# Kernel optimization log

Measured on AMD Instinct MI355X. Metric: run time of the kernel, lower is better.

## Reference

```python
import jax, jax.numpy as jnp
import numpy as np

H = 1024      # hidden_size
I = 2 * H     # intermediate_size (expand_factor=2)
N = 16        # ssm_state_size
K = 4         # conv_kernel
BATCH = 2
SEQ = 2048


def setup_inputs() -> dict:
    key = jax.random.key(0)
    k = jax.random.split(key, 6)
    x = jax.random.normal(k[0], (BATCH, SEQ, H), dtype=jnp.float32)
    # nn.Linear default init ~ U(-1/sqrt(fan_in), 1/sqrt(fan_in)); scale is fine for a reference
    W_in = jax.random.normal(k[1], (2 * I, H), dtype=jnp.float32) / np.sqrt(H)
    conv_w = jax.random.normal(k[2], (I, 1, K), dtype=jnp.float32) / np.sqrt(K)
    W_x = jax.random.normal(k[3], (2 * N + 1, I), dtype=jnp.float32) / np.sqrt(I)
    A_log = jax.random.normal(k[4], (I, N), dtype=jnp.float32)
    D = jnp.ones((I,), dtype=jnp.float32)
    W_out = jax.random.normal(k[5], (H, I), dtype=jnp.float32) / np.sqrt(I)
    return {"x": x, "W_in": W_in, "conv_w": conv_w, "W_x": W_x,
            "A_log": A_log, "D": D, "W_out": W_out}


def reference(x, W_in, conv_w, W_x, A_log, D, W_out):
    xz = jnp.einsum('bsh,ih->bsi', x, W_in)
    xp, z = jnp.split(xz, 2, axis=-1)
    # depthwise causal conv1d: pad left K-1 (torch pads both sides then slices [:S])
    xc = jax.lax.conv_general_dilated(
        xp.transpose(0, 2, 1),           # (B, I, S)
        conv_w,                          # (I, 1, K) = OIH with groups=I
        window_strides=(1,),
        padding=[(K - 1, 0)],
        feature_group_count=I,
        dimension_numbers=('NCH', 'OIH', 'NCH'),
    ).transpose(0, 2, 1)                 # (B, S, I)
    xc = jax.nn.silu(xc)
    # x_proj -> delta (1), B (N), C (N)
    xproj = jnp.einsum('bsi,pi->bsp', xc, W_x)   # (B,S,2N+1)
    delta = jax.nn.softplus(xproj[..., :1])       # (B,S,1)
    Bmat = xproj[..., 1:1 + N]                    # (B,S,N)
    Cmat = xproj[..., 1 + N:]                     # (B,S,N)
    A = -jnp.exp(A_log)                           # (I,N)
    # decay/states broadcast-reduce: (B,S,I,N) intermediates reduced over N
    decay = jnp.exp(delta[..., None] * A[None, None])            # (B,S,I,N)
    states = xc[..., None] * Bmat[:, :, None, :] * decay          # (B,S,I,N)
    y = jnp.sum(states * Cmat[:, :, None, :], axis=-1)            # (B,S,I)
    y = y + xc * D[None, None, :]
    return jnp.einsum('bsi,hi->bsh', y * jax.nn.silu(z), W_out)
```

## Files before the change

kernel.cpp:

```cpp
#include <hip/hip_runtime.h>

#define LOG2E 1.4426950408889634f

__device__ __forceinline__ float b2f(unsigned short u) {
    unsigned int v = ((unsigned int)u) << 16;
    return __builtin_bit_cast(float, v);
}
__device__ __forceinline__ unsigned short f2b(float f) {
    unsigned int u = __builtin_bit_cast(unsigned int, f);
    u += 0x7fffu + ((u >> 16) & 1u);
    return (unsigned short)(u >> 16);
}
__device__ __forceinline__ float fexp(float x) {
    return __builtin_amdgcn_exp2f(x * LOG2E);
}
__device__ __forceinline__ float silu_f(float x) {
    return x * __builtin_amdgcn_rcpf(1.0f + fexp(-x));
}

typedef const __attribute__((address_space(1))) unsigned int* gas_t;
typedef __attribute__((address_space(3))) unsigned int* las_t;
__device__ __forceinline__ void gl2lds16(const unsigned short* g, unsigned short* l) {
    __builtin_amdgcn_global_load_lds((gas_t)(const void*)g, (las_t)(void*)l, 16, 0, 0);
}

__global__ __launch_bounds__(256) void cvt_all_k(const float* __restrict__ x,
                                                 const float* __restrict__ W_in,
                                                 const float* __restrict__ W_out,
                                                 const float* __restrict__ W_x,
                                                 unsigned short* __restrict__ xb,
                                                 unsigned short* __restrict__ wib,
                                                 unsigned short* __restrict__ wob,
                                                 unsigned short* __restrict__ wxb) {
    int b = blockIdx.x;
    const float* src;
    unsigned short* dst;
    if (b < 4096)       { src = x;     dst = xb;  }
    else if (b < 8192)  { src = W_in;  dst = wib; b -= 4096; }
    else if (b < 10240) { src = W_out; dst = wob; b -= 8192; }
    else                { src = W_x;   dst = wxb; b -= 10240; }
    int i = b * 256 + threadIdx.x;
    float4 v = ((const float4*)src)[i];
    *(ushort4*)(dst + (size_t)i * 4) = make_ushort4(f2b(v.x), f2b(v.y), f2b(v.z), f2b(v.w));
}

typedef __bf16 bf16x8 __attribute__((ext_vector_type(8)));
typedef float  fx4    __attribute__((ext_vector_type(4)));
typedef int    ix4    __attribute__((ext_vector_type(4)));
union FragU { ix4 i; bf16x8 b; };

template <bool OUT_BF16>
__global__ __launch_bounds__(256) void gemm_bt(const unsigned short* __restrict__ A,
                                               const unsigned short* __restrict__ B,
                                               void* __restrict__ C, int N, int K) {
    __shared__ __align__(16) unsigned short sA[128 * 64];
    __shared__ __align__(16) unsigned short sB[128 * 64];
    const int tid  = threadIdx.x;
    const int lane = tid & 63, wave = tid >> 6;
    const int bm = blockIdx.y * 128, bn = blockIdx.x * 128;
    const int wm = (wave >> 1) * 64, wn = (wave & 1) * 64;
    const int row16 = lane & 15, quad = lane >> 4;
    const int srow = lane >> 3;
    const int sc16 = (lane & 7) ^ srow;
    const unsigned short* gA = A + (size_t)(bm + wave * 32 + srow) * K + sc16 * 8;
    const unsigned short* gB = B + (size_t)(bn + wave * 32 + srow) * K + sc16 * 8;
    unsigned short* lA = sA + (wave * 4) * 512;
    unsigned short* lB = sB + (wave * 4) * 512;
    fx4 acc[4][4] = {};

    for (int kt = 0; kt < K; kt += 64) {
#pragma unroll
        for (int it = 0; it < 4; ++it) {
            gl2lds16(gA + (size_t)it * 8 * K + kt, lA + it * 512);
            gl2lds16(gB + (size_t)it * 8 * K + kt, lB + it * 512);
        }
        __syncthreads();
#pragma unroll
        for (int kk = 0; kk < 64; kk += 32) {
            FragU af[4], bf[4];
#pragma unroll
            for (int t = 0; t < 4; ++t) {
                int ra = wm + t * 16 + row16;
                af[t].i = *(const ix4*)(sA + ra * 64 + ((quad + (kk >> 3)) ^ (ra & 7)) * 8);
            }
#pragma unroll
            for (int t = 0; t < 4; ++t) {
                int rb = wn + t * 16 + row16;
                bf[t].i = *(const ix4*)(sB + rb * 64 + ((quad + (kk >> 3)) ^ (rb & 7)) * 8);
            }
#pragma unroll
            for (int tm = 0; tm < 4; ++tm)
#pragma unroll
                for (int tn = 0; tn < 4; ++tn)
                    acc[tm][tn] = __builtin_amdgcn_mfma_f32_16x16x32_bf16(
                        af[tm].b, bf[tn].b, acc[tm][tn], 0, 0, 0);
        }
        __syncthreads();
    }
#pragma unroll
    for (int tm = 0; tm < 4; ++tm) {
        int row0 = bm + wm + tm * 16 + quad * 4;
#pragma unroll
        for (int tn = 0; tn < 4; ++tn) {
            int col = bn + wn + tn * 16 + row16;
#pragma unroll
            for (int r = 0; r < 4; ++r) {
                float v = acc[tm][tn][r];
                if (OUT_BF16)
                    ((unsigned short*)C)[(size_t)(row0 + r) * N + col] = f2b(v);
                else
                    ((float*)C)[(size_t)(row0 + r) * N + col] = v;
            }
        }
    }
}

__global__ __launch_bounds__(256) void gemm_bt_n64(const unsigned short* __restrict__ A,
                                                   const unsigned short* __restrict__ B,
                                                   float* __restrict__ C, int N, int K) {
    __shared__ __align__(16) unsigned short sA[128 * 64];
    __shared__ __align__(16) unsigned short sB[64 * 64];
    const int tid  = threadIdx.x;
    const int lane = tid & 63, wave = tid >> 6;
    const int bm = blockIdx.y * 128, bn = blockIdx.x * 64;
    const int wm = wave * 32;
    const int row16 = lane & 15, quad = lane >> 4;
    const int srow = lane >> 3;
    const int sc16 = (lane & 7) ^ srow;
    const unsigned short* gA = A + (size_t)(bm + wave * 32 + srow) * K + sc16 * 8;
    const unsigned short* gB = B + (size_t)(bn + wave * 16 + srow) * K + sc16 * 8;
    unsigned short* lA = sA + (wave * 4) * 512;
    unsigned short* lB = sB + (wave * 2) * 512;
    fx4 acc[2][4] = {};

    for (int kt = 0; kt < K; kt += 64) {
#pragma unroll
        for (int it = 0; it < 4; ++it)
            gl2lds16(gA + (size_t)it * 8 * K + kt, lA + it * 512);
#pragma unroll
        for (int it = 0; it < 2; ++it)
            gl2lds16(gB + (size_t)it * 8 * K + kt, lB + it * 512);
        __syncthreads();
#pragma unroll
        for (int kk = 0; kk < 64; kk += 32) {
            FragU af[2], bf[4];
#pragma unroll
            for (int t = 0; t < 2; ++t) {
                int ra = wm + t * 16 + row16;
                af[t].i = *(const ix4*)(sA + ra * 64 + ((quad + (kk >> 3)) ^ (ra & 7)) * 8);
            }
#pragma unroll
            for (int t = 0; t < 4; ++t) {
                int rb = t * 16 + row16;
                bf[t].i = *(const ix4*)(sB + rb * 64 + ((quad + (kk >> 3)) ^ (rb & 7)) * 8);
            }
#pragma unroll
            for (int tm = 0; tm < 2; ++tm)
#pragma unroll
                for (int tn = 0; tn < 4; ++tn)
                    acc[tm][tn] = __builtin_amdgcn_mfma_f32_16x16x32_bf16(
                        af[tm].b, bf[tn].b, acc[tm][tn], 0, 0, 0);
        }
        __syncthreads();
    }
#pragma unroll
    for (int tm = 0; tm < 2; ++tm) {
        int row0 = bm + wm + tm * 16 + quad * 4;
#pragma unroll
        for (int tn = 0; tn < 4; ++tn) {
            int col = bn + tn * 16 + row16;
#pragma unroll
            for (int r = 0; r < 4; ++r)
                C[(size_t)(row0 + r) * N + col] = acc[tm][tn][r];
        }
    }
}

__global__ __launch_bounds__(256) void fused_mid_k(const unsigned short* __restrict__ xz,
                                                   const float* __restrict__ cw,
                                                   const unsigned short* __restrict__ wxb,
                                                   const float* __restrict__ Alog,
                                                   const float* __restrict__ Dv,
                                                   unsigned short* __restrict__ y2) {
    __shared__ __align__(16) unsigned short sxc[16 * 2048];
    __shared__ float sX[4][16][49];
    __shared__ float sdg[16 * 17];
    const int tid  = threadIdx.x;
    const int lane = tid & 63, wave = tid >> 6;
    const int row16 = lane & 15, quad = lane >> 4;
    const int m0 = blockIdx.x * 16;

    {
        const float4* cw4 = (const float4*)cw;
        float w[8][4];
#pragma unroll
        for (int c = 0; c < 8; ++c) {
            float4 t4 = cw4[tid * 8 + c];
            w[c][0] = t4.x; w[c][1] = t4.y; w[c][2] = t4.z; w[c][3] = t4.w;
        }
        for (int j = 0; j < 16; ++j) {
            const int m = m0 + j, s = m & 2047;
            float acc[8] = {0, 0, 0, 0, 0, 0, 0, 0};
#pragma unroll
            for (int k = 0; k < 4; ++k) {
                if (s - 3 + k >= 0) {
                    const unsigned short* p = xz + (size_t)(m - 3 + k) * 4096 + tid * 8;
                    ushort4 a = *(const ushort4*)p;
                    ushort4 b = *(const ushort4*)(p + 4);
                    float v[8] = {b2f(a.x), b2f(a.y), b2f(a.z), b2f(a.w),
                                  b2f(b.x), b2f(b.y), b2f(b.z), b2f(b.w)};
#pragma unroll
                    for (int c = 0; c < 8; ++c) acc[c] += v[c] * w[c][k];
                }
            }
            unsigned short* q = sxc + j * 2048 + ((tid ^ (j & 7)) * 8);
            *(ushort4*)q       = make_ushort4(f2b(silu_f(acc[0])), f2b(silu_f(acc[1])),
                                              f2b(silu_f(acc[2])), f2b(silu_f(acc[3])));
            *(ushort4*)(q + 4) = make_ushort4(f2b(silu_f(acc[4])), f2b(silu_f(acc[5])),
                                              f2b(silu_f(acc[6])), f2b(silu_f(acc[7])));
        }
    }
    __syncthreads();

    {
        fx4 acc[3] = {};
        const unsigned short* bp = wxb + (size_t)row16 * 2048 + wave * 512 + quad * 8;
        const int cbase = wave * 64 + quad;
#pragma unroll 4
        for (int kk = 0; kk < 512; kk += 32) {
            FragU a, b0, b1, b2;
            int c16 = cbase + (kk >> 3);
            a.i  = *(const ix4*)(sxc + row16 * 2048 + ((c16 ^ (row16 & 7)) * 8));
            b0.i = *(const ix4*)(bp + kk);
            b1.i = *(const ix4*)(bp + 16 * 2048 + kk);
            b2.i = *(const ix4*)(bp + 32 * 2048 + kk);
            acc[0] = __builtin_amdgcn_mfma_f32_16x16x32_bf16(a.b, b0.b, acc[0], 0, 0, 0);
            acc[1] = __builtin_amdgcn_mfma_f32_16x16x32_bf16(a.b, b1.b, acc[1], 0, 0, 0);
            acc[2] = __builtin_amdgcn_mfma_f32_16x16x32_bf16(a.b, b2.b, acc[2], 0, 0, 0);
        }
#pragma unroll
        for (int t = 0; t < 3; ++t)
#pragma unroll
            for (int r = 0; r < 4; ++r)
                sX[wave][quad * 4 + r][t * 16 + row16] = acc[t][r];
    }
    __syncthreads();
    for (int idx = tid; idx < 272; idx += 256) {
        int rr = idx / 17, q = idx - rr * 17;
        float o;
        if (q == 0) {
            float v = sX[0][rr][0] + sX[1][rr][0] + sX[2][rr][0] + sX[3][rr][0];
            o = (v > 20.f) ? v : log1pf(fexp(v));
        } else {
            float bs = sX[0][rr][q]      + sX[1][rr][q]      + sX[2][rr][q]      + sX[3][rr][q];
            float cs = sX[0][rr][q + 16] + sX[1][rr][q + 16] + sX[2][rr][q + 16] + sX[3][rr][q + 16];
            o = bs * cs;
        }
        sdg[rr * 17 + q] = o;
    }
    __syncthreads();

#pragma unroll 1
    for (int p = 0; p < 2; ++p) {
        const int ch0 = p * 1024 + tid * 4;
        float a2[4][16];
#pragma unroll
        for (int c = 0; c < 4; ++c) {
            const float4* ar = (const float4*)(Alog + (size_t)(ch0 + c) * 16);
#pragma unroll
            for (int n4 = 0; n4 < 4; ++n4) {
                float4 t4 = ar[n4];
                a2[c][n4 * 4 + 0] = -fexp(t4.x) * LOG2E;
                a2[c][n4 * 4 + 1] = -fexp(t4.y) * LOG2E;
                a2[c][n4 * 4 + 2] = -fexp(t4.z) * LOG2E;
                a2[c][n4 * 4 + 3] = -fexp(t4.w) * LOG2E;
            }
        }
        float4 dvv = *(const float4*)(Dv + ch0);
        float dv[4] = {dvv.x, dvv.y, dvv.z, dvv.w};
        const int c16 = ch0 >> 3, sub = ch0 & 7;
        for (int j = 0; j < 16; ++j) {
            const int m = m0 + j;
            float delta = sdg[j * 17];
            float Gr[16];
#pragma unroll
            for (int n = 0; n < 16; ++n) Gr[n] = sdg[j * 17 + 1 + n];
            ushort4 xu = *(const ushort4*)(sxc + j * 2048 + ((c16 ^ (j & 7)) * 8) + sub);
            ushort4 zu = *(const ushort4*)(xz + (size_t)m * 4096 + 2048 + ch0);
            float xcv[4] = {b2f(xu.x), b2f(xu.y), b2f(xu.z), b2f(xu.w)};
            float zv[4]  = {b2f(zu.x), b2f(zu.y), b2f(zu.z), b2f(zu.w)};
            unsigned short ov[4];
#pragma unroll
            for (int c = 0; c < 4; ++c) {
                float ssum = 0.f;
#pragma unroll
                for (int n = 0; n < 16; ++n)
                    ssum += Gr[n] * __builtin_amdgcn_exp2f(delta * a2[c][n]);
                float y = xcv[c] * (dv[c] + ssum);
                ov[c] = f2b(y * silu_f(zv[c]));
            }
            *(ushort4*)(y2 + (size_t)m * 2048 + ch0) = make_ushort4(ov[0], ov[1], ov[2], ov[3]);
        }
    }
}

extern "C" void kernel_launch(void* const* d_in, const int* in_sizes, int n_in,
                              void* d_out, int out_size, void* d_ws, size_t ws_size,
                              hipStream_t stream) {
    const float* x      = (const float*)d_in[0];
    const float* W_in   = (const float*)d_in[1];
    const float* conv_w = (const float*)d_in[2];
    const float* W_x    = (const float*)d_in[3];
    const float* A_log  = (const float*)d_in[4];
    const float* Dvec   = (const float*)d_in[5];
    const float* W_out  = (const float*)d_in[6];

    char* ws = (char*)d_ws;
    unsigned short* xb  = (unsigned short*)(ws);
    unsigned short* wib = (unsigned short*)(ws + 8388608);
    unsigned short* wob = (unsigned short*)(ws + 16777216);
    unsigned short* xz  = (unsigned short*)(ws + 20971520);
    unsigned short* y2  = (unsigned short*)(ws + 54525952);
    unsigned short* wxb = (unsigned short*)(ws + 71303168);

    cvt_all_k<<<10306, 256, 0, stream>>>(x, W_in, W_out, W_x, xb, wib, wob, wxb);
    gemm_bt<true><<<dim3(32, 32), 256, 0, stream>>>(xb, wib, xz, 4096, 1024);
    fused_mid_k<<<256, 256, 0, stream>>>(xz, conv_w, wxb, A_log, Dvec, y2);
    gemm_bt_n64<<<dim3(16, 32), 256, 0, stream>>>(y2, wob, (float*)d_out, 1024, 2048);
}
```

Before: 217.9 us.

## Shrink fused mid kernel tile to 4 rows and launch 1024 blocks

The fused conv/x_proj/scan kernel now processes 4 tokens per block instead of 16, cutting LDS use and launching 1024 blocks so more blocks fit per CU and the GPU's CUs are filled (256 blocks was about one per CU). The conv input rows are loaded once into registers as a 7-row window and reused across the 4 outputs, and z loads are hoisted ahead of the scan loop. The tradeoff is that each block re-reads the full W_x matrix for the x_proj MFMA, with only 4 of 16 MFMA rows carrying useful data, and A_log exps are recomputed four times as often.

```diff
diff --git a/kernel.cpp b/kernel.cpp
--- a/kernel.cpp
+++ b/kernel.cpp
@@ -176,21 +176,30 @@
     }
 }
 
-__global__ __launch_bounds__(256) void fused_mid_k(const unsigned short* __restrict__ xz,
-                                                   const float* __restrict__ cw,
-                                                   const unsigned short* __restrict__ wxb,
-                                                   const float* __restrict__ Alog,
-                                                   const float* __restrict__ Dv,
-                                                   unsigned short* __restrict__ y2) {
-    __shared__ __align__(16) unsigned short sxc[16 * 2048];
+__global__ __launch_bounds__(256, 4) void fused_mid_k(const unsigned short* __restrict__ xz,
+                                                      const float* __restrict__ cw,
+                                                      const unsigned short* __restrict__ wxb,
+                                                      const float* __restrict__ Alog,
+                                                      const float* __restrict__ Dv,
+                                                      unsigned short* __restrict__ y2) {
+    __shared__ __align__(16) unsigned short sxc[4 * 2048];
     __shared__ float sX[4][16][49];
-    __shared__ float sdg[16 * 17];
+    __shared__ float sdg[4 * 17];
     const int tid  = threadIdx.x;
     const int lane = tid & 63, wave = tid >> 6;
     const int row16 = lane & 15, quad = lane >> 4;
-    const int m0 = blockIdx.x * 16;
+    const int m0 = blockIdx.x * 4;
 
     {
+        const int s0 = m0 & 2047;
+        ushort4 ua[7], ub[7];
+#pragma unroll
+        for (int t = 0; t < 7; ++t) {
+            int mr = (s0 - 3 + t >= 0) ? (m0 - 3 + t) : m0;
+            const unsigned short* p = xz + (size_t)mr * 4096 + tid * 8;
+            ua[t] = *(const ushort4*)p;
+            ub[t] = *(const ushort4*)(p + 4);
+        }
         const float4* cw4 = (const float4*)cw;
         float w[8][4];
 #pragma unroll
@@ -198,22 +207,28 @@
             float4 t4 = cw4[tid * 8 + c];
             w[c][0] = t4.x; w[c][1] = t4.y; w[c][2] = t4.z; w[c][3] = t4.w;
         }
-        for (int j = 0; j < 16; ++j) {
-            const int m = m0 + j, s = m & 2047;
-            float acc[8] = {0, 0, 0, 0, 0, 0, 0, 0};
-#pragma unroll
-            for (int k = 0; k < 4; ++k) {
-                if (s - 3 + k >= 0) {
-                    const unsigned short* p = xz + (size_t)(m - 3 + k) * 4096 + tid * 8;
-                    ushort4 a = *(const ushort4*)p;
-                    ushort4 b = *(const ushort4*)(p + 4);
-                    float v[8] = {b2f(a.x), b2f(a.y), b2f(a.z), b2f(a.w),
-                                  b2f(b.x), b2f(b.y), b2f(b.z), b2f(b.w)};
-#pragma unroll
-                    for (int c = 0; c < 8; ++c) acc[c] += v[c] * w[c][k];
-                }
-            }
-            unsigned short* q = sxc + j * 2048 + ((tid ^ (j & 7)) * 8);
+        float v[7][8];
+#pragma unroll
+        for (int t = 0; t < 7; ++t) {
+            bool valid = (s0 - 3 + t >= 0);
+            v[t][0] = valid ? b2f(ua[t].x) : 0.f;
+            v[t][1] = valid ? b2f(ua[t].y) : 0.f;
+            v[t][2] = valid ? b2f(ua[t].z) : 0.f;
+            v[t][3] = valid ? b2f(ua[t].w) : 0.f;
+            v[t][4] = valid ? b2f(ub[t].x) : 0.f;
+            v[t][5] = valid ? b2f(ub[t].y) : 0.f;
+            v[t][6] = valid ? b2f(ub[t].z) : 0.f;
+            v[t][7] = valid ? b2f(ub[t].w) : 0.f;
+        }
+#pragma unroll
+        for (int j = 0; j < 4; ++j) {
+            float acc[8];
+#pragma unroll
+            for (int c = 0; c < 8; ++c) {
+                acc[c] = v[j][c] * w[c][0] + v[j + 1][c] * w[c][1]
+                       + v[j + 2][c] * w[c][2] + v[j + 3][c] * w[c][3];
+            }
+            unsigned short* q = sxc + j * 2048 + ((tid ^ (j & 3)) * 8);
             *(ushort4*)q       = make_ushort4(f2b(silu_f(acc[0])), f2b(silu_f(acc[1])),
                                               f2b(silu_f(acc[2])), f2b(silu_f(acc[3])));
             *(ushort4*)(q + 4) = make_ushort4(f2b(silu_f(acc[4])), f2b(silu_f(acc[5])),
@@ -225,12 +240,13 @@
     {
         fx4 acc[3] = {};
         const unsigned short* bp = wxb + (size_t)row16 * 2048 + wave * 512 + quad * 8;
+        const int arow = row16 & 3;
         const int cbase = wave * 64 + quad;
 #pragma unroll 4
         for (int kk = 0; kk < 512; kk += 32) {
             FragU a, b0, b1, b2;
             int c16 = cbase + (kk >> 3);
-            a.i  = *(const ix4*)(sxc + row16 * 2048 + ((c16 ^ (row16 & 7)) * 8));
+            a.i  = *(const ix4*)(sxc + arow * 2048 + ((c16 ^ arow) * 8));
             b0.i = *(const ix4*)(bp + kk);
             b1.i = *(const ix4*)(bp + 16 * 2048 + kk);
             b2.i = *(const ix4*)(bp + 32 * 2048 + kk);
@@ -245,7 +261,7 @@
                 sX[wave][quad * 4 + r][t * 16 + row16] = acc[t][r];
     }
     __syncthreads();
-    for (int idx = tid; idx < 272; idx += 256) {
+    for (int idx = tid; idx < 68; idx += 256) {
         int rr = idx / 17, q = idx - rr * 17;
         float o;
         if (q == 0) {
@@ -263,6 +279,10 @@
 #pragma unroll 1
     for (int p = 0; p < 2; ++p) {
         const int ch0 = p * 1024 + tid * 4;
+        ushort4 zu[4];
+#pragma unroll
+        for (int j = 0; j < 4; ++j)
+            zu[j] = *(const ushort4*)(xz + (size_t)(m0 + j) * 4096 + 2048 + ch0);
         float a2[4][16];
 #pragma unroll
         for (int c = 0; c < 4; ++c) {
@@ -279,16 +299,16 @@
         float4 dvv = *(const float4*)(Dv + ch0);
         float dv[4] = {dvv.x, dvv.y, dvv.z, dvv.w};
         const int c16 = ch0 >> 3, sub = ch0 & 7;
-        for (int j = 0; j < 16; ++j) {
+#pragma unroll
+        for (int j = 0; j < 4; ++j) {
             const int m = m0 + j;
             float delta = sdg[j * 17];
             float Gr[16];
 #pragma unroll
             for (int n = 0; n < 16; ++n) Gr[n] = sdg[j * 17 + 1 + n];
-            ushort4 xu = *(const ushort4*)(sxc + j * 2048 + ((c16 ^ (j & 7)) * 8) + sub);
-            ushort4 zu = *(const ushort4*)(xz + (size_t)m * 4096 + 2048 + ch0);
+            ushort4 xu = *(const ushort4*)(sxc + j * 2048 + ((c16 ^ (j & 3)) * 8) + sub);
             float xcv[4] = {b2f(xu.x), b2f(xu.y), b2f(xu.z), b2f(xu.w)};
-            float zv[4]  = {b2f(zu.x), b2f(zu.y), b2f(zu.z), b2f(zu.w)};
+            float zv[4]  = {b2f(zu[j].x), b2f(zu[j].y), b2f(zu[j].z), b2f(zu[j].w)};
             unsigned short ov[4];
 #pragma unroll
             for (int c = 0; c < 4; ++c) {
@@ -325,6 +345,6 @@
 
     cvt_all_k<<<10306, 256, 0, stream>>>(x, W_in, W_out, W_x, xb, wib, wob, wxb);
     gemm_bt<true><<<dim3(32, 32), 256, 0, stream>>>(xb, wib, xz, 4096, 1024);
-    fused_mid_k<<<256, 256, 0, stream>>>(xz, conv_w, wxb, A_log, Dvec, y2);
+    fused_mid_k<<<1024, 256, 0, stream>>>(xz, conv_w, wxb, A_log, Dvec, y2);
     gemm_bt_n64<<<dim3(16, 32), 256, 0, stream>>>(y2, wob, (float*)d_out, 1024, 2048);
 }
```

Result: slower. 317.4 us (+45.7%).
